# Kernel optimization log

Hardware: AMD Instinct MI355X
Metric: run time of the kernel (lower is better)

## Reference

```python
import jax, jax.numpy as jnp
import numpy as np

SPATIAL_SHAPES = [(128, 128), (64, 64), (32, 32), (16, 16)]
D_MODEL = 256
N_HEADS = 8
N_LEVELS = 4
N_POINTS = 4
HEAD_DIM = D_MODEL // N_HEADS
B = 2
LEN_Q = sum(h * w for h, w in SPATIAL_SHAPES)  # 21760
LEN_IN = LEN_Q


def setup_inputs() -> dict:
    key = jax.random.key(0)
    ks = jax.random.split(key, 11)
    s = 1.0 / np.sqrt(D_MODEL).astype(np.float32)
    query = jax.random.normal(ks[0], (B, LEN_Q, D_MODEL), jnp.float32)
    reference_points = jax.random.uniform(ks[1], (B, LEN_Q, N_LEVELS, 2), jnp.float32)
    input_flatten = jax.random.normal(ks[2], (B, LEN_IN, D_MODEL), jnp.float32)
    W_off = jax.random.normal(ks[3], (D_MODEL, N_HEADS * N_LEVELS * N_POINTS * 2), jnp.float32) * s
    b_off = jnp.zeros((N_HEADS * N_LEVELS * N_POINTS * 2,), jnp.float32)
    W_attn = jax.random.normal(ks[4], (D_MODEL, N_HEADS * N_LEVELS * N_POINTS), jnp.float32) * s
    b_attn = jnp.zeros((N_HEADS * N_LEVELS * N_POINTS,), jnp.float32)
    W_val = jax.random.normal(ks[5], (D_MODEL, D_MODEL), jnp.float32) * s
    b_val = jnp.zeros((D_MODEL,), jnp.float32)
    W_out = jax.random.normal(ks[6], (D_MODEL, D_MODEL), jnp.float32) * s
    b_out = jnp.zeros((D_MODEL,), jnp.float32)
    return {"query": query, "reference_points": reference_points, "input_flatten": input_flatten,
            "W_off": W_off, "b_off": b_off, "W_attn": W_attn, "b_attn": b_attn,
            "W_val": W_val, "b_val": b_val, "W_out": W_out, "b_out": b_out}


def _ms_deform_core(value, sampling_locations, attention_weights):
    # value: (B, H, Dh, N_total); sampling_locations: (B, Lq, H, L, P, 2) in [0,1]
    # attention_weights: (B, Lq, H, L*P)
    Bv, Hn, Dh, _ = value.shape
    Lq = sampling_locations.shape[1]
    P = sampling_locations.shape[4]
    BN = Bv * Hn
    grids = 2.0 * sampling_locations - 1.0
    splits = np.cumsum([h * w for h, w in SPATIAL_SHAPES])[:-1].tolist()
    value_list = jnp.split(value, splits, axis=3)
    sampled_levels = []
    for lid, (Hh, Ww) in enumerate(SPATIAL_SHAPES):
        # (BN, H*W, Dh)
        val_flat = jnp.transpose(value_list[lid].reshape(BN, Dh, Hh * Ww), (0, 2, 1))
        # (BN, Lq, P, 2)
        g = jnp.transpose(grids[:, :, :, lid, :, :], (0, 2, 1, 3, 4)).reshape(BN, Lq, P, 2)
        ix = ((g[..., 0] + 1.0) * Ww - 1.0) / 2.0
        iy = ((g[..., 1] + 1.0) * Hh - 1.0) / 2.0
        ix0 = jnp.floor(ix).astype(jnp.int32)
        iy0 = jnp.floor(iy).astype(jnp.int32)
        ix1 = ix0 + 1
        iy1 = iy0 + 1
        fx = (ix - ix0.astype(ix.dtype))[..., None]
        fy = (iy - iy0.astype(iy.dtype))[..., None]

        def valid(yy, xx):
            return ((xx >= 0) & (xx < Ww) & (yy >= 0) & (yy < Hh)).astype(val_flat.dtype)[..., None]

        def gather(yy, xx):
            idx = (jnp.clip(yy, 0, Hh - 1) * Ww + jnp.clip(xx, 0, Ww - 1)).reshape(BN, Lq * P)
            out = jnp.take_along_axis(val_flat, idx[:, :, None], axis=1)
            return out.reshape(BN, Lq, P, Dh)

        v00 = gather(iy0, ix0) * valid(iy0, ix0)
        v01 = gather(iy0, ix1) * valid(iy0, ix1)
        v10 = gather(iy1, ix0) * valid(iy1, ix0)
        v11 = gather(iy1, ix1) * valid(iy1, ix1)
        sampled = ((1 - fx) * (1 - fy) * v00 + fx * (1 - fy) * v01
                   + (1 - fx) * fy * v10 + fx * fy * v11)  # (BN, Lq, P, Dh)
        sampled_levels.append(jnp.transpose(sampled, (0, 3, 1, 2)))  # (BN, Dh, Lq, P)
    # (BN, Dh, Lq, L*P)
    sv = jnp.stack(sampled_levels, axis=-2).reshape(BN, Dh, Lq, N_LEVELS * P)
    attn = jnp.transpose(attention_weights, (0, 2, 1, 3)).reshape(BN, 1, Lq, N_LEVELS * P)
    out = jnp.sum(sv * attn, axis=-1)  # (BN, Dh, Lq)
    out = out.reshape(Bv, Hn * Dh, Lq)
    return jnp.transpose(out, (0, 2, 1))  # (B, Lq, d_model)


def reference(query, reference_points, input_flatten, W_off, b_off, W_attn, b_attn, W_val, b_val, W_out, b_out):
    Bq, Lq, _ = query.shape
    Len_in = input_flatten.shape[1]
    value = input_flatten @ W_val + b_val  # (B, Len_in, d_model)
    offsets = (query @ W_off + b_off).reshape(Bq, Lq, N_HEADS, N_LEVELS, N_POINTS, 2)
    attn = jax.nn.softmax((query @ W_attn + b_attn).reshape(Bq, Lq, N_HEADS, N_LEVELS * N_POINTS), axis=-1)
    # normalizer is (W, H) per level
    offset_normalizer = jnp.asarray([[w, h] for h, w in SPATIAL_SHAPES], dtype=query.dtype)
    sampling_locations = (reference_points[:, :, None, :, None, :]
                          + offsets / offset_normalizer[None, None, None, :, None, :])
    value = jnp.transpose(value, (0, 2, 1)).reshape(Bq, N_HEADS, HEAD_DIM, Len_in)
    out = _ms_deform_core(value, sampling_locations, attn)
    return out @ W_out + b_out
```

## Files before the change

kernel.cpp:

```cpp
#include <hip/hip_runtime.h>
#include <hip/hip_bf16.h>
#include <hip/hip_fp16.h>
#include <type_traits>

#define B_    2
#define LQ_   21760
#define LEN_  21760
#define DM    256
#define NH    8
#define NL    4
#define NP    4
#define HD    32

#define WS_VAL   0u
#define WS_SAMP  22282240u
#define WS_OA    44564480u
#define WS_WT    77987840u

typedef __attribute__((ext_vector_type(4))) float f32x4;
typedef __attribute__((ext_vector_type(8))) short bf16x8;
typedef __attribute__((ext_vector_type(4))) unsigned int u32x4;
typedef __attribute__((ext_vector_type(2))) unsigned int u32x2;

__device__ __forceinline__ unsigned short f2bf(float v) {
    __hip_bfloat16 h = __float2bfloat16(v);
    return *reinterpret_cast<unsigned short*>(&h);
}
__device__ __forceinline__ unsigned int pk2bf(float a, float b) {
    return (unsigned int)f2bf(a) | ((unsigned int)f2bf(b) << 16);
}
__device__ __forceinline__ unsigned int pk2h(float a, float b) {
    __half2 h = __floats2half2_rn(a, b);
    union { __half2 h; unsigned int u; } c; c.h = h; return c.u;
}
__device__ __forceinline__ __half2 u2h2(unsigned int u) {
    union { unsigned int u; __half2 h; } c; c.u = u; return c.h;
}

__device__ __forceinline__ void gload16(u32x4& d, const char* p) {
    asm volatile("global_load_dwordx4 %0, %1, off" : "=v"(d) : "v"(p));
}

__global__ __launch_bounds__(256) void wt_cvt_all(const float* __restrict__ Wv,
                                                  const float* __restrict__ Wo,
                                                  const float* __restrict__ Wa,
                                                  const float* __restrict__ Wu,
                                                  unsigned short* __restrict__ wt) {
    const float* Ws[4] = {Wv, Wo, Wa, Wu};
    const int Ns[4] = {256, 256, 128, 256};
    const unsigned int dof[4] = {0u, 65536u, 131072u, 163840u};
    const int m = blockIdx.z;
    const int n0 = blockIdx.x * 16, k0 = blockIdx.y * 16;
    if (n0 >= Ns[m]) return;
    __shared__ float tile[16][17];
    const int tx = threadIdx.x & 15, ty = threadIdx.x >> 4;
    tile[ty][tx] = Ws[m][(size_t)(k0 + ty) * Ns[m] + n0 + tx];
    __syncthreads();
    wt[dof[m] + (size_t)(n0 + ty) * 256 + k0 + tx] = f2bf(tile[tx][ty]);
}

__global__ __launch_bounds__(256) void gemm_pre(const float* __restrict__ inpf,
                                                const float* __restrict__ query,
                                                const unsigned short* __restrict__ Wt_val,
                                                const unsigned short* __restrict__ Wt_oa,
                                                const float* __restrict__ b_val,
                                                const float* __restrict__ b_off,
                                                const float* __restrict__ b_attn,
                                                unsigned short* __restrict__ val_h,
                                                unsigned short* __restrict__ oa_h) {
    __shared__ unsigned short As[128 * 32];
    __shared__ unsigned short Bs[128 * 32];
    const int t = threadIdx.x;
    const int wv = t >> 6;
    const int ln = t & 63;
    const int job = (blockIdx.x >= 2);
    const int n0 = (job ? (blockIdx.x - 2) : blockIdx.x) * 128;
    const int m0 = blockIdx.y * 128;
    const float* A = job ? query : inpf;
    const unsigned short* Bt = job ? Wt_oa : Wt_val;
    const int K = 256;
    const int wm = (wv & 1) * 64;
    const int wn = (wv >> 1) * 64;
    const int lrow = ln & 15;
    const int kq = ln >> 4;

    f32x4 acc[4][4] = {};

    for (int k0 = 0; k0 < K; k0 += 32) {
#pragma unroll
        for (int c = 0; c < 4; ++c) {
            const int i = t + c * 256;
            const int row = i >> 3;
            const int kq4 = (i & 7) * 4;
            f32x4 v = *(const f32x4*)&A[(size_t)(m0 + row) * K + k0 + kq4];
            uint2 p = make_uint2(pk2bf(v.x, v.y), pk2bf(v.z, v.w));
            *(uint2*)((char*)As + row * 64 + kq4 * 2) = p;
        }
#pragma unroll
        for (int c = 0; c < 2; ++c) {
            const int o = c * 4096 + t * 16;
            const int row = o >> 6;
            const int ke = (o & 63) >> 1;
            const unsigned short* gb = Bt + (size_t)(n0 + row) * K + k0 + ke;
            __builtin_amdgcn_global_load_lds(
                (const __attribute__((address_space(1))) void*)gb,
                (__attribute__((address_space(3))) void*)((char*)Bs + o), 16, 0, 0);
        }
        __syncthreads();

        bf16x8 af[4], bfr[4];
#pragma unroll
        for (int i = 0; i < 4; ++i) {
            af[i]  = *(const bf16x8*)((char*)As + (wm + i * 16 + lrow) * 64 + kq * 16);
            bfr[i] = *(const bf16x8*)((char*)Bs + (wn + i * 16 + lrow) * 64 + kq * 16);
        }
#pragma unroll
        for (int i = 0; i < 4; ++i)
#pragma unroll
            for (int j = 0; j < 4; ++j)
                acc[i][j] = __builtin_amdgcn_mfma_f32_16x16x32_bf16(af[i], bfr[j], acc[i][j], 0, 0, 0);
        __syncthreads();
    }

    const int b = m0 / LQ_;
#pragma unroll
    for (int j = 0; j < 4; ++j) {
        const int n = n0 + wn + j * 16 + lrow;
        const float bb = job ? ((n < 256) ? b_off[n] : b_attn[n - 256]) : b_val[n];
#pragma unroll
        for (int i = 0; i < 4; ++i) {
            const int mrow = m0 + wm + i * 16 + kq * 4;
#pragma unroll
            for (int r = 0; r < 4; ++r) {
                const float v = acc[i][j][r] + bb;
                const unsigned short hv = (unsigned short)__half_as_ushort(__float2half(v));
                if (job) {
                    oa_h[(size_t)(mrow + r) * 384 + n] = hv;
                } else {
                    const int pix = (mrow + r) - b * LQ_;
                    const int h = n >> 5, c = n & 31;
                    val_h[((size_t)(b * NH + h) * LQ_ + pix) * HD + c] = hv;
                }
            }
        }
    }
}

__global__ __launch_bounds__(256) void gemm_out(const unsigned short* __restrict__ Ab,
                                                const unsigned short* __restrict__ Bt,
                                                const float* __restrict__ bias,
                                                float* __restrict__ C) {
    __shared__ unsigned short As[128 * 32];
    __shared__ unsigned short Bs[128 * 32];
    const int t = threadIdx.x;
    const int wv = t >> 6;
    const int ln = t & 63;
    const int n0 = blockIdx.x * 128;
    const int m0 = blockIdx.y * 128;
    const int N = 256, K = 256;
    const int wm = (wv & 1) * 64;
    const int wn = (wv >> 1) * 64;
    const int lrow = ln & 15;
    const int kq = ln >> 4;

    f32x4 acc[4][4] = {};

    for (int k0 = 0; k0 < K; k0 += 32) {
#pragma unroll
        for (int c = 0; c < 2; ++c) {
            const int o = c * 4096 + t * 16;
            const int row = o >> 6;
            const int ke = (o & 63) >> 1;
            const unsigned short* ga = Ab + (size_t)(m0 + row) * K + k0 + ke;
            const unsigned short* gb = Bt + (size_t)(n0 + row) * K + k0 + ke;
            __builtin_amdgcn_global_load_lds(
                (const __attribute__((address_space(1))) void*)ga,
                (__attribute__((address_space(3))) void*)((char*)As + o), 16, 0, 0);
            __builtin_amdgcn_global_load_lds(
                (const __attribute__((address_space(1))) void*)gb,
                (__attribute__((address_space(3))) void*)((char*)Bs + o), 16, 0, 0);
        }
        __syncthreads();

        bf16x8 af[4], bfr[4];
#pragma unroll
        for (int i = 0; i < 4; ++i) {
            af[i]  = *(const bf16x8*)((char*)As + (wm + i * 16 + lrow) * 64 + kq * 16);
            bfr[i] = *(const bf16x8*)((char*)Bs + (wn + i * 16 + lrow) * 64 + kq * 16);
        }
#pragma unroll
        for (int i = 0; i < 4; ++i)
#pragma unroll
            for (int j = 0; j < 4; ++j)
                acc[i][j] = __builtin_amdgcn_mfma_f32_16x16x32_bf16(af[i], bfr[j], acc[i][j], 0, 0, 0);
        __syncthreads();
    }

#pragma unroll
    for (int j = 0; j < 4; ++j) {
        const int n = n0 + wn + j * 16 + lrow;
        const float bb = bias[n];
#pragma unroll
        for (int i = 0; i < 4; ++i) {
            const int mrow = m0 + wm + i * 16 + kq * 4;
#pragma unroll
            for (int r = 0; r < 4; ++r)
                C[(size_t)(mrow + r) * N + n] = acc[i][j][r] + bb;
        }
    }
}

#define QB6 32

#define MSDA_VMWAIT(n) { asm volatile("s_waitcnt vmcnt(" #n ")" ::: "memory"); \
                         __builtin_amdgcn_sched_barrier(0); }

#define MSDA_ISSUE(i) u32x4 va_##i, vc_##i; { \
    const u32x2 xy = *(const u32x2*)&s_pkw[wb ^ ((i) << 2)]; \
    gload16(va_##i, vbase + (size_t)xy[0] * 64); \
    gload16(vc_##i, vbase + (size_t)xy[1] * 64); }

#define MSDA_CONSUME(i) { \
    const u32x2 zw = *(const u32x2*)&s_pkw[(wb ^ ((i) << 2)) + 2]; \
    const __half2 w0 = u2h2(__builtin_amdgcn_perm(zw[0], zw[0], wsel)); \
    const __half2 w1 = u2h2(__builtin_amdgcn_perm(zw[1], zw[1], wsel)); \
    ah0 = __hfma2(w0, u2h2(va_##i[0]), ah0); \
    ah1 = __hfma2(w0, u2h2(va_##i[1]), ah1); \
    ah2 = __hfma2(w0, u2h2(va_##i[2]), ah2); \
    ah3 = __hfma2(w0, u2h2(va_##i[3]), ah3); \
    ah0 = __hfma2(w1, u2h2(vc_##i[0]), ah0); \
    ah1 = __hfma2(w1, u2h2(vc_##i[1]), ah1); \
    ah2 = __hfma2(w1, u2h2(vc_##i[2]), ah2); \
    ah3 = __hfma2(w1, u2h2(vc_##i[3]), ah3); }

#define MSDA_FLUSH() { \
    float2 f0 = __half22float2(ah0); facc0 += f0.x; facc1 += f0.y; ah0 = u2h2(0u); \
    float2 f1 = __half22float2(ah1); facc2 += f1.x; facc3 += f1.y; ah1 = u2h2(0u); \
    float2 f2 = __half22float2(ah2); facc4 += f2.x; facc5 += f2.y; ah2 = u2h2(0u); \
    float2 f3 = __half22float2(ah3); facc6 += f3.x; facc7 += f3.y; ah3 = u2h2(0u); }

__global__ __launch_bounds__(256) void msda_sample8(const unsigned short* __restrict__ value,
                                                    const unsigned short* __restrict__ oa,
                                                    const float* __restrict__ refp,
                                                    unsigned short* __restrict__ samp,
                                                    const int jbase) {
    __shared__ __align__(16) char smem[9216];
    unsigned int* s_pkw = (unsigned int*)smem;
    float* s_off   = (float*)smem;
    float* s_logit = (float*)(smem + 4096);
    float* s_aw    = (float*)(smem + 6144);
    float* s_ref   = (float*)(smem + 8192);

    const int t = threadIdx.x;
    const int j = blockIdx.x + jbase;
    const int h = j & 7;
    const int bqc = j >> 3;
    const int b = (bqc >= 680);
    const int q0 = (bqc - b * 680) * QB6;
    const int bq0 = b * LQ_ + q0;

    {
        const int q = t >> 3, c = t & 7;
        const unsigned short* oab = oa + (size_t)(bq0 + q) * 384;
        u32x2 r0 = __builtin_nontemporal_load((const u32x2*)(oab + h * 32) + c);
        float2 f0 = __half22float2(u2h2(r0.x));
        float2 f1 = __half22float2(u2h2(r0.y));
        f32x4 o0 = {f0.x, f0.y, f1.x, f1.y};
        ((f32x4*)s_off)[q * 8 + c] = o0;
        unsigned int r1 = __builtin_nontemporal_load((const unsigned int*)(oab + 256 + h * 16) + c);
        float2 g0 = __half22float2(u2h2(r1));
        ((float2*)s_logit)[q * 8 + c] = make_float2(g0.x, g0.y);
        s_ref[q * 8 + c] = __builtin_nontemporal_load(refp + (size_t)(bq0 + q) * 8 + c);
    }
    __syncthreads();

    if (t < 32) {
        const float* lg = s_logit + t * 16;
        float m = -1e30f;
#pragma unroll
        for (int i = 0; i < 16; ++i) m = fmaxf(m, lg[i]);
        float e[16], s = 0.f;
#pragma unroll
        for (int i = 0; i < 16; ++i) { e[i] = __expf(lg[i] - m); s += e[i]; }
        const float inv = 1.f / s;
#pragma unroll
        for (int i = 0; i < 16; ++i) s_aw[t * 16 + i] = e[i] * inv;
    }
    __syncthreads();

    uint4 ent[2];
    int wrd[2];
    {
        const int Wls[4] = {128, 64, 32, 16};
        const int Hls[4] = {128, 64, 32, 16};
        const int st_[4] = {0, 16384, 20480, 21504};
#pragma unroll
        for (int ii = 0; ii < 2; ++ii) {
            const int s = t * 2 + ii;
            const int q = s >> 4;
            const int lp = s & 15;
            const int l = lp >> 2;
            const int Wl = Wls[l], Hl = Hls[l], base = st_[l];
            const float ix = s_ref[q * 8 + l * 2]     * (float)Wl - 0.5f + s_off[q * 32 + lp * 2];
            const float iy = s_ref[q * 8 + l * 2 + 1] * (float)Hl - 0.5f + s_off[q * 32 + lp * 2 + 1];
            const float fix = floorf(ix), fiy = floorf(iy);
            const int x0 = (int)fix, y0 = (int)fiy;
            const float fx = ix - fix, fy = iy - fiy;
            int sx; float wl, wr;
            if (x0 < 0)            { sx = 0;      wl = (x0 == -1) ? fx : 0.f;        wr = 0.f; }
            else if (x0 >= Wl - 1) { sx = Wl - 2; wl = 0.f; wr = (x0 == Wl - 1) ? (1.f - fx) : 0.f; }
            else                   { sx = x0;     wl = 1.f - fx;                     wr = fx; }
            const float g0 = ((y0 >= 0) & (y0 < Hl)) ? (1.f - fy) : 0.f;
            const float g1 = ((y0 + 1 >= 0) & (y0 + 1 < Hl)) ? fy : 0.f;
            const int cy0 = min(max(y0, 0), Hl - 1);
            const int cy1 = min(max(y0 + 1, 0), Hl - 1);
            const float aw = s_aw[q * 16 + lp];
            ent[ii].x = (unsigned int)(base + cy0 * Wl + sx);
            ent[ii].y = (unsigned int)(base + cy1 * Wl + sx);
            ent[ii].z = pk2h(aw * wl * g0, aw * wr * g0);
            ent[ii].w = pk2h(aw * wl * g1, aw * wr * g1);
            wrd[ii] = q * 64 + ((lp ^ (q & 7)) << 2);
        }
    }
    __syncthreads();

#pragma unroll
    for (int ii = 0; ii < 2; ++ii)
        *(uint4*)&s_pkw[wrd[ii]] = ent[ii];
    __syncthreads();

    const int lane = t & 63;
    const int wv = t >> 6;
    const int ql = lane >> 3;
    const int q = wv * 8 + ql;
    const int dg = lane & 7;
    const char* vbase = (const char*)(value + ((size_t)(b * NH + h) * LQ_) * HD) + dg * 16;
    const unsigned int wsel = (dg < 4) ? 0x01000100u : 0x03020302u;
    const int wb = q * 64 + (ql << 2);

    float facc0 = 0.f, facc1 = 0.f, facc2 = 0.f, facc3 = 0.f;
    float facc4 = 0.f, facc5 = 0.f, facc6 = 0.f, facc7 = 0.f;
    __half2 ah0 = u2h2(0u), ah1 = u2h2(0u), ah2 = u2h2(0u), ah3 = u2h2(0u);

    MSDA_ISSUE(0)  MSDA_ISSUE(1)  MSDA_ISSUE(2)  MSDA_ISSUE(3)
    MSDA_ISSUE(4)  MSDA_ISSUE(5)  MSDA_ISSUE(6)  MSDA_ISSUE(7)
    MSDA_VMWAIT(8)
    MSDA_ISSUE(8)  MSDA_ISSUE(9)  MSDA_ISSUE(10) MSDA_ISSUE(11)
    MSDA_CONSUME(0) MSDA_CONSUME(1) MSDA_CONSUME(2) MSDA_CONSUME(3)
    MSDA_FLUSH()
    MSDA_VMWAIT(8)
    MSDA_ISSUE(12) MSDA_ISSUE(13) MSDA_ISSUE(14) MSDA_ISSUE(15)
    MSDA_CONSUME(4) MSDA_CONSUME(5) MSDA_CONSUME(6) MSDA_CONSUME(7)
    MSDA_FLUSH()
    MSDA_VMWAIT(8)
    MSDA_CONSUME(8) MSDA_CONSUME(9) MSDA_CONSUME(10) MSDA_CONSUME(11)
    MSDA_FLUSH()
    MSDA_VMWAIT(0)
    MSDA_CONSUME(12) MSDA_CONSUME(13) MSDA_CONSUME(14) MSDA_CONSUME(15)
    MSDA_FLUSH()

    facc0 += __shfl_xor(facc0, 4);
    facc1 += __shfl_xor(facc1, 4);
    facc2 += __shfl_xor(facc2, 4);
    facc3 += __shfl_xor(facc3, 4);
    facc4 += __shfl_xor(facc4, 4);
    facc5 += __shfl_xor(facc5, 4);
    facc6 += __shfl_xor(facc6, 4);
    facc7 += __shfl_xor(facc7, 4);

    if (dg < 4) {
        u32x4 o;
        o.x = pk2bf(facc0, facc1);
        o.y = pk2bf(facc2, facc3);
        o.z = pk2bf(facc4, facc5);
        o.w = pk2bf(facc6, facc7);
        __builtin_nontemporal_store(o, (u32x4*)(samp + (size_t)(bq0 + q) * 256 + h * HD + dg * 8));
    }
}

extern "C" void kernel_launch(void* const* d_in, const int* in_sizes, int n_in,
                              void* d_out, int out_size, void* d_ws, size_t ws_size,
                              hipStream_t stream) {
    const float* query  = (const float*)d_in[0];
    const float* refp   = (const float*)d_in[1];
    const float* inpf   = (const float*)d_in[2];
    const float* W_off  = (const float*)d_in[3];
    const float* b_off  = (const float*)d_in[4];
    const float* W_attn = (const float*)d_in[5];
    const float* b_attn = (const float*)d_in[6];
    const float* W_val  = (const float*)d_in[7];
    const float* b_val  = (const float*)d_in[8];
    const float* W_out  = (const float*)d_in[9];
    const float* b_out  = (const float*)d_in[10];
    float* out = (float*)d_out;

    char* ws = (char*)d_ws;
    unsigned short* val_h   = (unsigned short*)(ws + WS_VAL);
    unsigned short* samp_bf = (unsigned short*)(ws + WS_SAMP);
    unsigned short* oa_h    = (unsigned short*)(ws + WS_OA);
    unsigned short* wt      = (unsigned short*)(ws + WS_WT);
    unsigned short* Wt_val  = wt;
    unsigned short* Wt_oa   = wt + 65536;
    unsigned short* Wt_out  = wt + 163840;

    const int M = B_ * LQ_;
    const int JH = B_ * NH * (LQ_ / QB6) / 2;

    wt_cvt_all<<<dim3(16, 16, 4), 256, 0, stream>>>(W_val, W_off, W_attn, W_out, wt);

    gemm_pre<<<dim3(5, M / 128), 256, 0, stream>>>(
        inpf, query, Wt_val, Wt_oa, b_val, b_off, b_attn, val_h, oa_h);

    msda_sample8<<<dim3(JH), 256, 0, stream>>>(val_h, oa_h, refp, samp_bf, 0);
    msda_sample8<<<dim3(JH), 256, 0, stream>>>(val_h, oa_h, refp, samp_bf, JH);

    gemm_out<<<dim3(2, M / 128), 256, 0, stream>>>(samp_bf, Wt_out, b_out, out);
}
```

Before: 283.8 us.

## Software-pipeline gemm_pre with register-prefetched A and double-buffered B tiles

Rewrites the pre-projection GEMM so the next K-slice of the fp32 A operand is prefetched into registers and the B tile is loaded into a second LDS buffer while the current slice is computed. Explicit vmcnt/lgkmcnt waits and s_barrier replace the two __syncthreads per iteration. The grid is flattened to 1D, and block indices are remapped so consecutive workgroups land on the same XCD for better L2 locality. This costs more registers and LDS, and the hand-written wait counts and XCD mapping constants are fragile.

```diff
diff --git a/kernel.cpp b/kernel.cpp
--- a/kernel.cpp
+++ b/kernel.cpp
@@ -39,6 +39,12 @@
 
 __device__ __forceinline__ void gload16(u32x4& d, const char* p) {
     asm volatile("global_load_dwordx4 %0, %1, off" : "=v"(d) : "v"(p));
+}
+
+__device__ __forceinline__ uint2 cvt4bf(const u32x4& a) {
+    union { unsigned u; float f; } x0, x1, x2, x3;
+    x0.u = a[0]; x1.u = a[1]; x2.u = a[2]; x3.u = a[3];
+    return make_uint2(pk2bf(x0.f, x1.f), pk2bf(x2.f, x3.f));
 }
 
 __global__ __launch_bounds__(256) void wt_cvt_all(const float* __restrict__ Wv,
@@ -59,68 +65,121 @@
     wt[dof[m] + (size_t)(n0 + ty) * 256 + k0 + tx] = f2bf(tile[tx][ty]);
 }
 
-__global__ __launch_bounds__(256) void gemm_pre(const float* __restrict__ inpf,
-                                                const float* __restrict__ query,
-                                                const unsigned short* __restrict__ Wt_val,
-                                                const unsigned short* __restrict__ Wt_oa,
-                                                const float* __restrict__ b_val,
-                                                const float* __restrict__ b_off,
-                                                const float* __restrict__ b_attn,
-                                                unsigned short* __restrict__ val_h,
-                                                unsigned short* __restrict__ oa_h) {
+#define GP_ISSUE_A(S) { \
+    gload16(a##S##0, pA0); gload16(a##S##1, pA1); \
+    gload16(a##S##2, pA2); gload16(a##S##3, pA3); \
+    pA0 += 128; pA1 += 128; pA2 += 128; pA3 += 128; }
+
+#define GP_ISSUE_B(DST) { \
+    __builtin_amdgcn_global_load_lds( \
+        (const __attribute__((address_space(1))) void*)pB0, \
+        (__attribute__((address_space(3))) void*)((DST) + o0), 16, 0, 0); \
+    __builtin_amdgcn_global_load_lds( \
+        (const __attribute__((address_space(1))) void*)pB1, \
+        (__attribute__((address_space(3))) void*)((DST) + o1), 16, 0, 0); \
+    pB0 += 32; pB1 += 32; }
+
+#define GP_WRITE_A(S) { \
+    *(uint2*)as0 = cvt4bf(a##S##0); \
+    *(uint2*)as1 = cvt4bf(a##S##1); \
+    *(uint2*)as2 = cvt4bf(a##S##2); \
+    *(uint2*)as3 = cvt4bf(a##S##3); }
+
+#define GP_COMPUTE(BSRC) { \
+    bf16x8 af[4], bfr[4]; \
+    _Pragma("unroll") \
+    for (int i = 0; i < 4; ++i) { \
+        af[i]  = *(const bf16x8*)((const char*)As + (wm + i * 16 + lrow) * 64 + kq * 16); \
+        bfr[i] = *(const bf16x8*)((BSRC) + (wn + i * 16 + lrow) * 64 + kq * 16); \
+    } \
+    _Pragma("unroll") \
+    for (int i = 0; i < 4; ++i) \
+        _Pragma("unroll") \
+        for (int jj = 0; jj < 4; ++jj) \
+            acc[i][jj] = __builtin_amdgcn_mfma_f32_16x16x32_bf16(af[i], bfr[jj], acc[i][jj], 0, 0, 0); }
+
+#define GP_STEP(ISS, USE, VM, BCUR, BNXT) { \
+    GP_ISSUE_A(ISS) \
+    GP_ISSUE_B(BNXT) \
+    asm volatile("s_waitcnt vmcnt(" #VM ")" ::: "memory"); \
+    __builtin_amdgcn_sched_barrier(0); \
+    GP_WRITE_A(USE) \
+    asm volatile("s_waitcnt lgkmcnt(0)" ::: "memory"); \
+    __builtin_amdgcn_s_barrier(); \
+    __builtin_amdgcn_sched_barrier(0); \
+    GP_COMPUTE(BCUR) \
+    __builtin_amdgcn_s_barrier(); }
+
+__global__ __launch_bounds__(256) void gemm_pre2(const float* __restrict__ inpf,
+                                                 const float* __restrict__ query,
+                                                 const unsigned short* __restrict__ Wt_val,
+                                                 const unsigned short* __restrict__ Wt_oa,
+                                                 const float* __restrict__ b_val,
+                                                 const float* __restrict__ b_off,
+                                                 const float* __restrict__ b_attn,
+                                                 unsigned short* __restrict__ val_h,
+                                                 unsigned short* __restrict__ oa_h) {
     __shared__ unsigned short As[128 * 32];
-    __shared__ unsigned short Bs[128 * 32];
+    __shared__ unsigned short Bs0[128 * 32];
+    __shared__ unsigned short Bs1[128 * 32];
     const int t = threadIdx.x;
     const int wv = t >> 6;
     const int ln = t & 63;
-    const int job = (blockIdx.x >= 2);
-    const int n0 = (job ? (blockIdx.x - 2) : blockIdx.x) * 128;
-    const int m0 = blockIdx.y * 128;
+
+    const int i0 = blockIdx.x;
+    const int xcd = i0 & 7, off = i0 >> 3;
+    const int wg = (xcd < 4 ? xcd * 213 : 852 + (xcd - 4) * 212) + off;
+    const int by = wg / 5, bx = wg - by * 5;
+
+    const int job = (bx >= 2);
+    const int n0 = (job ? (bx - 2) : bx) * 128;
+    const int m0 = by * 128;
     const float* A = job ? query : inpf;
     const unsigned short* Bt = job ? Wt_oa : Wt_val;
-    const int K = 256;
     const int wm = (wv & 1) * 64;
     const int wn = (wv >> 1) * 64;
     const int lrow = ln & 15;
     const int kq = ln >> 4;
 
+    const int rA = t >> 3;
+    const int kq4 = (t & 7) * 4;
+    const char* pA0 = (const char*)(A + (size_t)(m0 + rA) * 256 + kq4);
+    const char* pA1 = pA0 + 32 * 256 * 4;
+    const char* pA2 = pA1 + 32 * 256 * 4;
+    const char* pA3 = pA2 + 32 * 256 * 4;
+    char* as0 = (char*)As + rA * 64 + kq4 * 2;
+    char* as1 = as0 + 32 * 64;
+    char* as2 = as1 + 32 * 64;
+    char* as3 = as2 + 32 * 64;
+
+    const int o0 = t * 16, o1 = 4096 + t * 16;
+    const int brow0 = o0 >> 6, ke0 = (o0 & 63) >> 1;
+    const int brow1 = o1 >> 6, ke1 = (o1 & 63) >> 1;
+    const unsigned short* pB0 = Bt + (size_t)(n0 + brow0) * 256 + ke0;
+    const unsigned short* pB1 = Bt + (size_t)(n0 + brow1) * 256 + ke1;
+    char* bsc0 = (char*)Bs0;
+    char* bsc1 = (char*)Bs1;
+
     f32x4 acc[4][4] = {};
-
-    for (int k0 = 0; k0 < K; k0 += 32) {
-#pragma unroll
-        for (int c = 0; c < 4; ++c) {
-            const int i = t + c * 256;
-            const int row = i >> 3;
-            const int kq4 = (i & 7) * 4;
-            f32x4 v = *(const f32x4*)&A[(size_t)(m0 + row) * K + k0 + kq4];
-            uint2 p = make_uint2(pk2bf(v.x, v.y), pk2bf(v.z, v.w));
-            *(uint2*)((char*)As + row * 64 + kq4 * 2) = p;
-        }
-#pragma unroll
-        for (int c = 0; c < 2; ++c) {
-            const int o = c * 4096 + t * 16;
-            const int row = o >> 6;
-            const int ke = (o & 63) >> 1;
-            const unsigned short* gb = Bt + (size_t)(n0 + row) * K + k0 + ke;
-            __builtin_amdgcn_global_load_lds(
-                (const __attribute__((address_space(1))) void*)gb,
-                (__attribute__((address_space(3))) void*)((char*)Bs + o), 16, 0, 0);
-        }
-        __syncthreads();
-
-        bf16x8 af[4], bfr[4];
-#pragma unroll
-        for (int i = 0; i < 4; ++i) {
-            af[i]  = *(const bf16x8*)((char*)As + (wm + i * 16 + lrow) * 64 + kq * 16);
-            bfr[i] = *(const bf16x8*)((char*)Bs + (wn + i * 16 + lrow) * 64 + kq * 16);
-        }
-#pragma unroll
-        for (int i = 0; i < 4; ++i)
-#pragma unroll
-            for (int j = 0; j < 4; ++j)
-                acc[i][j] = __builtin_amdgcn_mfma_f32_16x16x32_bf16(af[i], bfr[j], acc[i][j], 0, 0, 0);
-        __syncthreads();
-    }
+    u32x4 aA0, aA1, aA2, aA3, aB0, aB1, aB2, aB3;
+
+    GP_ISSUE_A(A)
+    GP_ISSUE_B(bsc0)
+
+    GP_STEP(B, A, 6, bsc0, bsc1)
+    GP_STEP(A, B, 6, bsc1, bsc0)
+    GP_STEP(B, A, 6, bsc0, bsc1)
+    GP_STEP(A, B, 6, bsc1, bsc0)
+    GP_STEP(B, A, 6, bsc0, bsc1)
+    GP_STEP(A, B, 6, bsc1, bsc0)
+    GP_STEP(B, A, 6, bsc0, bsc1)
+    asm volatile("s_waitcnt vmcnt(0)" ::: "memory");
+    __builtin_amdgcn_sched_barrier(0);
+    GP_WRITE_A(B)
+    asm volatile("s_waitcnt lgkmcnt(0)" ::: "memory");
+    __builtin_amdgcn_s_barrier();
+    __builtin_amdgcn_sched_barrier(0);
+    GP_COMPUTE(bsc1)
 
     const int b = m0 / LQ_;
 #pragma unroll
@@ -408,7 +467,7 @@
 
     wt_cvt_all<<<dim3(16, 16, 4), 256, 0, stream>>>(W_val, W_off, W_attn, W_out, wt);
 
-    gemm_pre<<<dim3(5, M / 128), 256, 0, stream>>>(
+    gemm_pre2<<<dim3(5 * (M / 128)), 256, 0, stream>>>(
         inpf, query, Wt_val, Wt_oa, b_val, b_off, b_attn, val_h, oa_h);
 
     msda_sample8<<<dim3(JH), 256, 0, stream>>>(val_h, oa_h, refp, samp_bf, 0);
```

Measured after the change: 276.4 us. 2.6% less time.
